# Kernel optimization log

Measured on AMD Instinct MI355X. Metric: run time of the kernel, lower is better.

The kernel has to match this reference:

```python
import jax, jax.numpy as jnp
import numpy as np

N = 10240
E = N * 32
D = 128
K = 1        # k of KMISCoarsening
EPS = 0.5    # lazy random-walk epsilon
CHUNK = 256  # SpMM column chunk


def setup_inputs() -> dict:
    key = jax.random.key(0)
    k1, k2, k3, k4, k5 = jax.random.split(key, 5)
    x = jax.random.normal(k1, (N, D), dtype=jnp.float32)
    edge_index = jax.random.randint(k2, (2, E), 0, N, dtype=jnp.int32)
    edge_attr = jax.random.uniform(k3, (E,), dtype=jnp.float32)
    # ordering='random' -> rank is a random permutation of node ids
    rank = jax.random.permutation(k4, N).astype(jnp.int32)
    # one uniform per node for multinomial (inverse-CDF) cluster sampling
    u = jax.random.uniform(k5, (N,), dtype=jnp.float32)
    return {"x": x, "edge_attr": edge_attr, "u": u,
            "edge_index": edge_index, "rank": rank}


def maximal_k_independent_set(row, col, rank, k, n):
    """Blelloch-style parallel maximal k-independent set (k-mis-pool sample.py)."""
    def prop_min(mr):
        for _ in range(k):  # k-hop min-rank propagation
            nb = jnp.full((n,), n, dtype=mr.dtype).at[col].min(mr[row])
            mr = jnp.minimum(nb, mr)
        return mr

    def prop_max(m):
        for _ in range(k):  # k-hop coverage propagation
            nb = jnp.zeros((n,), dtype=m.dtype).at[col].max(m[row])
            m = jnp.maximum(nb, m)
        return m

    def cond(state):
        _, mask, _ = state
        return ~jnp.all(mask)

    def body(state):
        mis, mask, mr = state
        mr = prop_min(mr)
        mis = mis | (rank == mr)
        mask = prop_max(mis.astype(jnp.int32)).astype(bool)
        mr = jnp.where(mask, jnp.int32(n), rank)
        return mis, mask, mr

    init = (jnp.zeros((n,), bool), jnp.zeros((n,), bool), rank)
    mis, _, _ = jax.lax.while_loop(cond, body, init)
    return mis


def spmm(row, col, val, dense):
    """sparse(COO) @ dense, chunked over dense columns to bound memory."""
    n, m = dense.shape
    chunks = jnp.moveaxis(dense.reshape(n, m // CHUNK, CHUNK), 1, 0)

    def f(Dj):  # (n, CHUNK)
        return jnp.zeros((n, CHUNK), dense.dtype).at[row].add(val[:, None] * Dj[col])

    out = jax.lax.map(f, chunks)  # (m//CHUNK, n, CHUNK)
    return jnp.moveaxis(out, 0, 1).reshape(n, m)


def reference(x, edge_attr, u, edge_index, rank):
    n, d = x.shape
    row, col = edge_index[0], edge_index[1]

    # --- k-MIS sampling ---
    mis = maximal_k_independent_set(row, col, rank, K, n)

    # --- lazy random walk: rw = (1-eps)*D^-1 A, diag += eps ---
    deg = jnp.zeros((n,), x.dtype).at[row].add(edge_attr)
    rw_val = (1.0 - EPS) * edge_attr / jnp.where(deg == 0, 1.0, deg)[row]
    sl = jnp.arange(n, dtype=row.dtype)
    rw_row = jnp.concatenate([row, sl])
    rw_col = jnp.concatenate([col, sl])
    rw_v = jnp.concatenate([rw_val, jnp.full((n,), EPS, x.dtype)])

    # --- C = rw^k @ I[:, mis]; coarse dim padded to n (non-MIS cols are zero) ---
    C = jnp.diag(mis.astype(x.dtype))
    for _ in range(K):
        C = spmm(rw_row, rw_col, rw_v, C)
    rowsum = C.sum(axis=1, keepdims=True)  # normalize_dim(c_mat)
    C = C / jnp.where(rowsum == 0, 1.0, rowsum)

    # --- sample_partition_matrix: per-row multinomial via inverse CDF ---
    cdf = jnp.cumsum(C, axis=1)
    cluster = jnp.argmax(cdf > u[:, None] * cdf[:, -1:], axis=1)  # (n,) int

    # --- pool: out = normalize_dim(P^T) @ x  == per-cluster mean ---
    counts = jnp.zeros((n,), x.dtype).at[cluster].add(1.0)
    out = jnp.zeros((n, d), x.dtype).at[cluster].add(x)
    out = out / jnp.maximum(counts, 1.0)[:, None]

    # --- coarsen: adj_c = P^T @ (adj @ P), padded dense (n, n) ---
    adj_c = jnp.zeros((n, n), x.dtype).at[cluster[row], cluster[col]].add(edge_attr)

    return out, adj_c, mis, cluster
```

## Files before the change

### kernel.cpp

```cpp
#include <hip/hip_runtime.h>
#include <cstddef>

#define NN 10240
#define NE (NN * 32)
#define DD 128
#define MIS_ITERS 40
#define MAXD 128

#define OFF_OUT ((size_t)0)
#define OFF_ADJ ((size_t)NN * DD)
#define OFF_MIS (OFF_ADJ + (size_t)NN * (size_t)NN)
#define OFF_CL  (OFF_MIS + (size_t)NN)

__global__ void k_init(int* rcnt, int* cursor, int* misA, int* covA, int* nbA,
                       int* unc, int* one_, float* cntF) {
  int v = blockIdx.x * blockDim.x + threadIdx.x;
  if (v < NN) {
    rcnt[v] = 0; cursor[v] = 0; misA[v] = 0; covA[v] = 0; nbA[v] = NN;
    cntF[v] = 0.0f;
  }
  if (v < MIS_ITERS) unc[v] = 0;
  if (v == 0) one_[0] = 1;
}

__global__ void k_hist(const int* __restrict__ rowA, int* __restrict__ rcnt) {
  int e = blockIdx.x * blockDim.x + threadIdx.x;
  if (e < NE) atomicAdd(&rcnt[rowA[e]], 1);
}

__global__ void k_scan(const int* __restrict__ rcnt, int* __restrict__ rptr) {
  __shared__ int part[1024];
  int t = threadIdx.x;
  int local[10];
  int sum = 0;
  for (int k = 0; k < 10; k++) { local[k] = sum; sum += rcnt[t * 10 + k]; }
  part[t] = sum;
  __syncthreads();
  for (int off = 1; off < 1024; off <<= 1) {
    int v = (t >= off) ? part[t - off] : 0;
    __syncthreads();
    part[t] += v;
    __syncthreads();
  }
  int base = (t == 0) ? 0 : part[t - 1];
  for (int k = 0; k < 10; k++) rptr[t * 10 + k] = base + local[k];
  if (t == 1023) rptr[NN] = part[1023];
}

__global__ void k_fill(const int* __restrict__ rowA, const int* __restrict__ rptr,
                       int* __restrict__ cursor, int* __restrict__ ebuf) {
  int e = blockIdx.x * blockDim.x + threadIdx.x;
  if (e >= NE) return;
  int r = rowA[e];
  int p = atomicAdd(&cursor[r], 1);
  ebuf[rptr[r] + p] = e;
}

__device__ inline unsigned long long shfl_xor_u64(unsigned long long x, int m) {
  int lo = (int)(unsigned)(x & 0xFFFFFFFFull);
  int hi = (int)(unsigned)(x >> 32);
  lo = __shfl_xor(lo, m);
  hi = __shfl_xor(hi, m);
  return (((unsigned long long)(unsigned)hi) << 32) | (unsigned)lo;
}

__global__ void k_rowprep(int* __restrict__ ebuf, const int* __restrict__ rptr,
                          const int* __restrict__ colA, const float* __restrict__ attr,
                          float* __restrict__ degA) {
  int lane = threadIdx.x & 63;
  int v = blockIdx.x * (blockDim.x >> 6) + (threadIdx.x >> 6);
  if (v >= NN) return;
  int s = rptr[v], t = rptr[v + 1];
  int d = t - s;

  if (d > MAXD) {
    if (lane == 0) {
      for (int i = s + 1; i < t; i++) {
        int key = ebuf[i];
        int j = i - 1;
        while (j >= s && ebuf[j] > key) { ebuf[j + 1] = ebuf[j]; j--; }
        ebuf[j + 1] = key;
      }
      float dsum = 0.0f;
      for (int i = s; i < t; i++) dsum += attr[ebuf[i]];
      degA[v] = dsum;
      for (int i = s + 1; i < t; i++) {
        int key = ebuf[i];
        int kc = colA[key];
        int j = i - 1;
        while (j >= s && colA[ebuf[j]] > kc) { ebuf[j + 1] = ebuf[j]; j--; }
        ebuf[j + 1] = key;
      }
    }
    return;
  }

  unsigned e0 = (lane < d) ? (unsigned)ebuf[s + lane] : 0xFFFFFFFFu;
  unsigned e1 = (lane + 64 < d) ? (unsigned)ebuf[s + 64 + lane] : 0xFFFFFFFFu;

  for (int k = 2; k <= 128; k <<= 1) {
    for (int j = k >> 1; j >= 1; j >>= 1) {
      if (j >= 64) {
        unsigned lo = min(e0, e1), hi = max(e0, e1);
        e0 = lo; e1 = hi;
      } else {
        unsigned p0 = (unsigned)__shfl_xor((int)e0, j);
        unsigned p1 = (unsigned)__shfl_xor((int)e1, j);
        bool low = ((lane & j) == 0);
        bool up0 = ((lane & k) == 0);
        bool up1 = (((lane + 64) & k) == 0);
        e0 = (low == up0) ? min(e0, p0) : max(e0, p0);
        e1 = (low == up1) ? min(e1, p1) : max(e1, p1);
      }
    }
  }

  float a0 = (lane < d) ? attr[e0] : 0.0f;
  float a1 = (lane + 64 < d) ? attr[e1] : 0.0f;
  float dsum = 0.0f;
  for (int i = 0; i < d; i++) {
    float ai = (i < 64) ? __shfl(a0, i) : __shfl(a1, i - 64);
    dsum += ai;
  }
  if (lane == 0) degA[v] = dsum;

  unsigned long long k0 = (lane < d)
      ? ((((unsigned long long)(unsigned)colA[e0]) << 19) | (unsigned long long)e0)
      : ~0ull;
  unsigned long long k1 = (lane + 64 < d)
      ? ((((unsigned long long)(unsigned)colA[e1]) << 19) | (unsigned long long)e1)
      : ~0ull;
  for (int k = 2; k <= 128; k <<= 1) {
    for (int j = k >> 1; j >= 1; j >>= 1) {
      if (j >= 64) {
        unsigned long long lo = (k0 < k1) ? k0 : k1;
        unsigned long long hi = (k0 < k1) ? k1 : k0;
        k0 = lo; k1 = hi;
      } else {
        unsigned long long p0 = shfl_xor_u64(k0, j);
        unsigned long long p1 = shfl_xor_u64(k1, j);
        bool low = ((lane & j) == 0);
        bool up0 = ((lane & k) == 0);
        bool up1 = (((lane + 64) & k) == 0);
        unsigned long long n0 = (low == up0) ? ((k0 < p0) ? k0 : p0) : ((k0 < p0) ? p0 : k0);
        unsigned long long n1 = (low == up1) ? ((k1 < p1) ? k1 : p1) : ((k1 < p1) ? p1 : k1);
        k0 = n0; k1 = n1;
      }
    }
  }
  if (lane < d)      ebuf[s + lane]      = (int)(k0 & 0x7FFFFull);
  if (lane + 64 < d) ebuf[s + 64 + lane] = (int)(k1 & 0x7FFFFull);
}

__global__ void k_emin(const int* __restrict__ gate, const int* __restrict__ rowA,
                       const int* __restrict__ colA, const int* __restrict__ covA,
                       const int* __restrict__ rank, int* __restrict__ nbA) {
  if (*gate == 0) return;
  int e = blockIdx.x * blockDim.x + threadIdx.x;
  if (e >= NE) return;
  int r = rowA[e];
  if (covA[r]) return;
  atomicMin(&nbA[colA[e]], rank[r]);
}

__global__ void k_node1(const int* __restrict__ gate, const int* __restrict__ rank,
                        int* __restrict__ nbA, int* __restrict__ misA,
                        int* __restrict__ covA, int* __restrict__ unc_i) {
  if (*gate == 0) return;
  int v = blockIdx.x * blockDim.x + threadIdx.x;
  if (v >= NN) return;
  int cov = covA[v];
  int nb = nbA[v];
  nbA[v] = NN;
  int mr0 = cov ? NN : rank[v];
  int m = min(nb, mr0);
  int mi = misA[v];
  if (rank[v] == m) mi = 1;
  misA[v] = mi;
  int c2 = cov | mi;
  covA[v] = c2;
  if (!c2) atomicAdd(unc_i, 1);
}

__global__ void k_ecov(const int* __restrict__ gate, const int* __restrict__ rowA,
                       const int* __restrict__ colA, const int* __restrict__ misA,
                       int* __restrict__ covA) {
  if (*gate == 0) return;
  int e = blockIdx.x * blockDim.x + threadIdx.x;
  if (e >= NE) return;
  if (misA[rowA[e]]) covA[colA[e]] = 1;
}

template <int MODE>
__device__ float walk_row(int v, int s, int t, const int* __restrict__ ebuf,
                          const int* __restrict__ colA, const float* __restrict__ attr,
                          const int* __restrict__ misA, float dsafe, int misv,
                          float rs_safe, float thr, int* outc) {
  int i = s;
  int sp = misv;
  float cum = 0.0f;
  while (i < t || sp) {
    int bc;
    if (i < t) {
      int c = colA[ebuf[i]];
      bc = (sp && v <= c) ? v : c;
    } else {
      bc = v;
    }
    float b = 0.0f;
    while (i < t) {
      int e = ebuf[i];
      int c = colA[e];
      if (c != bc) break;
      if (misA[c]) b += (0.5f * attr[e]) / dsafe;
      i++;
    }
    if (sp && bc == v) { b += 0.5f; sp = 0; }
    if (MODE == 0) {
      cum += b;
    } else {
      float nv = b / rs_safe;
      cum += nv;
      if (MODE == 2 && cum > thr) { *outc = bc; return cum; }
    }
  }
  return cum;
}

__global__ void k_cluster(const int* __restrict__ rptr, const int* __restrict__ ebuf,
                          const int* __restrict__ colA, const float* __restrict__ attr,
                          const float* __restrict__ degA, const int* __restrict__ misA,
                          const float* __restrict__ u, int* __restrict__ clA) {
  int v = blockIdx.x * blockDim.x + threadIdx.x;
  if (v >= NN) return;
  int s = rptr[v], t = rptr[v + 1];
  float degv = degA[v];
  float dsafe = (degv == 0.0f) ? 1.0f : degv;
  int misv = misA[v];
  int dummy = 0;
  float rs = walk_row<0>(v, s, t, ebuf, colA, attr, misA, dsafe, misv, 1.0f, 0.0f, &dummy);
  float rs_safe = (rs == 0.0f) ? 1.0f : rs;
  float last = walk_row<1>(v, s, t, ebuf, colA, attr, misA, dsafe, misv, rs_safe, 0.0f, &dummy);
  float thr = u[v] * last;
  int c = 0;
  walk_row<2>(v, s, t, ebuf, colA, attr, misA, dsafe, misv, rs_safe, thr, &c);
  clA[v] = c;
}

__global__ void k_final(const int* __restrict__ misA, const int* __restrict__ clA,
                        float* __restrict__ outF, float* __restrict__ cntF) {
  int v = blockIdx.x * blockDim.x + threadIdx.x;
  if (v >= NN) return;
  outF[OFF_MIS + v] = misA[v] ? 1.0f : 0.0f;
  outF[OFF_CL + v] = (float)clA[v];
  atomicAdd(&cntF[clA[v]], 1.0f);
}

__global__ void k_pool(const float* __restrict__ x, const int* __restrict__ clA,
                       float* __restrict__ outF) {
  int idx = blockIdx.x * blockDim.x + threadIdx.x;
  if (idx >= NN * DD) return;
  int v = idx >> 7;
  int d = idx & 127;
  atomicAdd(&outF[OFF_OUT + (size_t)clA[v] * DD + d], x[idx]);
}

__global__ void k_div(const float* __restrict__ cntF, float* __restrict__ outF) {
  int idx = blockIdx.x * blockDim.x + threadIdx.x;
  if (idx >= NN * DD) return;
  int v = idx >> 7;
  outF[OFF_OUT + idx] = outF[OFF_OUT + idx] / fmaxf(cntF[v], 1.0f);
}

__global__ void k_adj(const int* __restrict__ rowA, const int* __restrict__ colA,
                      const float* __restrict__ attr, const int* __restrict__ clA,
                      float* __restrict__ outF) {
  int e = blockIdx.x * blockDim.x + threadIdx.x;
  if (e >= NE) return;
  int cr = clA[rowA[e]];
  int cc = clA[colA[e]];
  atomicAdd(&outF[OFF_ADJ + (size_t)cr * NN + cc], attr[e]);
}

extern "C" void kernel_launch(void* const* d_in, const int* in_sizes, int n_in,
                              void* d_out, int out_size, void* d_ws, size_t ws_size,
                              hipStream_t stream) {
  const float* x    = (const float*)d_in[0];
  const float* attr = (const float*)d_in[1];
  const float* u    = (const float*)d_in[2];
  const int*   ei   = (const int*)d_in[3];
  const int*   rank = (const int*)d_in[4];
  const int* rowA = ei;
  const int* colA = ei + NE;
  float* outF = (float*)d_out;

  int* rcnt   = (int*)d_ws;
  int* cursor = rcnt + NN;
  int* rptr   = cursor + NN;
  int* ebuf   = rptr + NN + 1;
  int* misA   = ebuf + NE;
  int* covA   = misA + NN;
  int* nbA    = covA + NN;
  int* clA    = nbA + NN;
  int* unc    = clA + NN;
  int* one_   = unc + MIS_ITERS;
  float* degA = (float*)(one_ + 1);
  float* cntF = degA + NN;

  hipMemsetAsync(d_out, 0, (size_t)out_size * sizeof(float), stream);

  dim3 blk(256);
  dim3 gN((NN + 255) / 256);
  dim3 gE((NE + 255) / 256);
  dim3 gND((NN * DD + 255) / 256);
  dim3 gR((NN + 3) / 4);

  k_init<<<gN, blk, 0, stream>>>(rcnt, cursor, misA, covA, nbA, unc, one_, cntF);
  k_hist<<<gE, blk, 0, stream>>>(rowA, rcnt);
  k_scan<<<1, 1024, 0, stream>>>(rcnt, rptr);
  k_fill<<<gE, blk, 0, stream>>>(rowA, rptr, cursor, ebuf);
  k_rowprep<<<gR, blk, 0, stream>>>(ebuf, rptr, colA, attr, degA);

  for (int i = 0; i < MIS_ITERS; i++) {
    const int* gate = (i == 0) ? one_ : (unc + (i - 1));
    k_emin<<<gE, blk, 0, stream>>>(gate, rowA, colA, covA, rank, nbA);
    k_node1<<<gN, blk, 0, stream>>>(gate, rank, nbA, misA, covA, unc + i);
    k_ecov<<<gE, blk, 0, stream>>>(gate, rowA, colA, misA, covA);
  }

  k_cluster<<<gN, blk, 0, stream>>>(rptr, ebuf, colA, attr, degA, misA, u, clA);
  k_final<<<gN, blk, 0, stream>>>(misA, clA, outF, cntF);
  k_pool<<<gND, blk, 0, stream>>>(x, clA, outF);
  k_div<<<gND, blk, 0, stream>>>(cntF, outF);
  k_adj<<<gE, blk, 0, stream>>>(rowA, colA, attr, clA, outF);
}
```

Measured before the change: 954.4 us.

## Fuse MIS iterations into one cooperative persistent kernel with grid syncs

Replaces the 120 per-iteration MIS kernel launches with a single cooperative kernel that loops over iterations using grid-wide syncs and exits early once no uncovered nodes remain. Also skips atomicMin for already-covered targets and avoids redundant cover stores, and shrinks k_cluster's block size to 64 threads. This aims to cut launch and gate-check overhead, at the cost of relying on cooperative launch residency (512x256 blocks) and grid-sync latency, with a fallback to the old path.

```diff
diff --git a/kernel.cpp b/kernel.cpp
--- a/kernel.cpp
+++ b/kernel.cpp
@@ -1,11 +1,16 @@
 #include <hip/hip_runtime.h>
+#include <hip/hip_cooperative_groups.h>
 #include <cstddef>
+
+namespace cg = cooperative_groups;
 
 #define NN 10240
 #define NE (NN * 32)
 #define DD 128
 #define MIS_ITERS 40
 #define MAXD 128
+#define MIS_BLOCKS 512
+#define MIS_TPB 256
 
 #define OFF_OUT ((size_t)0)
 #define OFF_ADJ ((size_t)NN * DD)
@@ -152,6 +157,48 @@
   if (lane + 64 < d) ebuf[s + 64 + lane] = (int)(k1 & 0x7FFFFull);
 }
 
+__global__ void k_mis(const int* __restrict__ rowA, const int* __restrict__ colA,
+                      const int* __restrict__ rank, int* __restrict__ misA,
+                      int* __restrict__ covA, int* __restrict__ nbA,
+                      int* __restrict__ unc) {
+  cg::grid_group grid = cg::this_grid();
+  const int tid = blockIdx.x * blockDim.x + threadIdx.x;
+  const int nthr = gridDim.x * blockDim.x;
+  for (int it = 0; it < MIS_ITERS; ++it) {
+    for (int e = tid; e < NE; e += nthr) {
+      int r = rowA[e];
+      if (covA[r]) continue;
+      int c = colA[e];
+      if (covA[c]) continue;
+      atomicMin(&nbA[c], rank[r]);
+    }
+    grid.sync();
+    for (int v = tid; v < NN; v += nthr) {
+      int cov = covA[v];
+      int nb = nbA[v];
+      nbA[v] = NN;
+      int mr0 = cov ? NN : rank[v];
+      int m = min(nb, mr0);
+      int mi = misA[v];
+      if (rank[v] == m) mi = 1;
+      misA[v] = mi;
+      int c2 = cov | mi;
+      covA[v] = c2;
+      if (!c2) atomicAdd(&unc[it], 1);
+    }
+    grid.sync();
+    for (int e = tid; e < NE; e += nthr) {
+      if (misA[rowA[e]]) {
+        int c = colA[e];
+        if (!covA[c]) covA[c] = 1;
+      }
+    }
+    grid.sync();
+    if (__hip_atomic_load(&unc[it], __ATOMIC_RELAXED, __HIP_MEMORY_SCOPE_AGENT) == 0)
+      break;
+  }
+}
+
 __global__ void k_emin(const int* __restrict__ gate, const int* __restrict__ rowA,
                        const int* __restrict__ colA, const int* __restrict__ covA,
                        const int* __restrict__ rank, int* __restrict__ nbA) {
@@ -160,7 +207,9 @@
   if (e >= NE) return;
   int r = rowA[e];
   if (covA[r]) return;
-  atomicMin(&nbA[colA[e]], rank[r]);
+  int c = colA[e];
+  if (covA[c]) return;
+  atomicMin(&nbA[c], rank[r]);
 }
 
 __global__ void k_node1(const int* __restrict__ gate, const int* __restrict__ rank,
@@ -188,7 +237,10 @@
   if (*gate == 0) return;
   int e = blockIdx.x * blockDim.x + threadIdx.x;
   if (e >= NE) return;
-  if (misA[rowA[e]]) covA[colA[e]] = 1;
+  if (misA[rowA[e]]) {
+    int c = colA[e];
+    if (!covA[c]) covA[c] = 1;
+  }
 }
 
 template <int MODE>
@@ -314,6 +366,8 @@
   dim3 gE((NE + 255) / 256);
   dim3 gND((NN * DD + 255) / 256);
   dim3 gR((NN + 3) / 4);
+  dim3 blkC(64);
+  dim3 gC((NN + 63) / 64);
 
   k_init<<<gN, blk, 0, stream>>>(rcnt, cursor, misA, covA, nbA, unc, one_, cntF);
   k_hist<<<gE, blk, 0, stream>>>(rowA, rcnt);
@@ -321,14 +375,25 @@
   k_fill<<<gE, blk, 0, stream>>>(rowA, rptr, cursor, ebuf);
   k_rowprep<<<gR, blk, 0, stream>>>(ebuf, rptr, colA, attr, degA);
 
-  for (int i = 0; i < MIS_ITERS; i++) {
-    const int* gate = (i == 0) ? one_ : (unc + (i - 1));
-    k_emin<<<gE, blk, 0, stream>>>(gate, rowA, colA, covA, rank, nbA);
-    k_node1<<<gN, blk, 0, stream>>>(gate, rank, nbA, misA, covA, unc + i);
-    k_ecov<<<gE, blk, 0, stream>>>(gate, rowA, colA, misA, covA);
-  }
-
-  k_cluster<<<gN, blk, 0, stream>>>(rptr, ebuf, colA, attr, degA, misA, u, clA);
+  {
+    const int* rA = rowA; const int* cA = colA; const int* rk = rank;
+    int* mA = misA; int* cvA = covA; int* nA = nbA; int* uA = unc;
+    void* args[] = {(void*)&rA, (void*)&cA, (void*)&rk,
+                    (void*)&mA, (void*)&cvA, (void*)&nA, (void*)&uA};
+    hipError_t ce = hipLaunchCooperativeKernel((const void*)k_mis,
+                                               dim3(MIS_BLOCKS), dim3(MIS_TPB),
+                                               args, 0, stream);
+    if (ce != hipSuccess) {
+      for (int i = 0; i < MIS_ITERS; i++) {
+        const int* gate = (i == 0) ? one_ : (unc + (i - 1));
+        k_emin<<<gE, blk, 0, stream>>>(gate, rowA, colA, covA, rank, nbA);
+        k_node1<<<gN, blk, 0, stream>>>(gate, rank, nbA, misA, covA, unc + i);
+        k_ecov<<<gE, blk, 0, stream>>>(gate, rowA, colA, misA, covA);
+      }
+    }
+  }
+
+  k_cluster<<<gC, blkC, 0, stream>>>(rptr, ebuf, colA, attr, degA, misA, u, clA);
   k_final<<<gN, blk, 0, stream>>>(misA, clA, outF, cntF);
   k_pool<<<gND, blk, 0, stream>>>(x, clA, outF);
   k_div<<<gND, blk, 0, stream>>>(cntF, outF);
```

Result: slower. 1.744 ms (+82.7%).
